# Kernel optimization log

Measured on AMD Instinct MI355X. Metric: run time of the kernel, lower is better.

Reference implementation:

```python
import jax, jax.numpy as jnp
import numpy as np

BATCH, SEQ, D_IN, D_HID, D_OUT = 256, 512, 128, 128, 128


def setup_inputs() -> dict:
    key = jax.random.key(0)
    ks = jax.random.split(key, 10)
    def xavier(k, shape):
        std = (2.0 / (shape[0] + shape[1])) ** 0.5
        return jax.random.normal(k, shape, dtype=jnp.float32) * std
    return {
        "x": jax.random.normal(ks[0], (BATCH, SEQ, D_IN), dtype=jnp.float32),
        "x2i": xavier(ks[1], (D_IN, D_HID)),
        "x2f": xavier(ks[2], (D_IN, D_HID)),
        "x2g": xavier(ks[3], (D_IN, D_HID)),
        "x2o": xavier(ks[4], (D_IN, D_HID)),
        "h2i": xavier(ks[5], (D_HID, D_HID)),
        "h2f": xavier(ks[6], (D_HID, D_HID)),
        "h2g": xavier(ks[7], (D_HID, D_HID)),
        "h2o": xavier(ks[8], (D_HID, D_HID)),
        "w_out": xavier(ks[9], (D_HID, D_OUT)),
    }


def reference(x, x2i, x2f, x2g, x2o, h2i, h2f, h2g, h2o, w_out):
    batch = x.shape[0]
    hid = h2i.shape[0]
    # Precompute input projections for all timesteps (same math, hoisted out
    # of the recurrence): [B, S, 4H] -> time-major [S, B, 4H]
    wx = jnp.concatenate([x2i, x2f, x2g, x2o], axis=1)       # [D_IN, 4H]
    wh = jnp.concatenate([h2i, h2f, h2g, h2o], axis=1)       # [H, 4H]
    xg = jnp.einsum("bsi,ik->sbk", x, wx)                    # [S, B, 4H]

    def step(carry, xg_t):
        c, h = carry
        gates = xg_t + h @ wh                                # [B, 4H]
        i = jax.nn.sigmoid(gates[:, 0 * hid:1 * hid])
        f = jax.nn.sigmoid(gates[:, 1 * hid:2 * hid])
        g = jnp.tanh(gates[:, 2 * hid:3 * hid])
        o = jax.nn.sigmoid(gates[:, 3 * hid:4 * hid])
        c = f * c + i * g
        h = o * jnp.tanh(c)
        return (c, h), None

    c0 = jnp.zeros((batch, hid), dtype=x.dtype)
    h0 = jnp.zeros((batch, hid), dtype=x.dtype)
    (c_T, h_T), _ = jax.lax.scan(step, (c0, h0), xg)
    return h_T @ w_out
```

## Files before the change

### kernel.cpp

```cpp
#include <hip/hip_runtime.h>

typedef unsigned int u32;
typedef __fp16 half2_t __attribute__((ext_vector_type(2)));
typedef __fp16 half8_t __attribute__((ext_vector_type(8)));
typedef float  f32x4   __attribute__((ext_vector_type(4)));

#define DIN 128
#define DH  128
#define SEQL 512
#define NBATCH 256
#define NC  512
#define TC  64
#define NCHUNK (SEQL/TC)

#define LDS_HOFF 65536
#define LDS_TOTAL (65536 + 512)

__device__ __forceinline__ u32 pk2(float a, float b) {
  half2_t h = __builtin_amdgcn_cvt_pkrtz(a, b);
  return __builtin_bit_cast(u32, h);
}

__device__ __forceinline__ float fexp2(float x) {
#if defined(__has_builtin) && __has_builtin(__builtin_amdgcn_exp2f)
  return __builtin_amdgcn_exp2f(x);
#else
  return __builtin_exp2f(x);
#endif
}

#define MF(A, B, C) __builtin_amdgcn_mfma_f32_16x16x32_f16( \
    __builtin_bit_cast(half8_t, A), __builtin_bit_cast(half8_t, B), C, 0, 0, 0)

__global__ void pack_w(const float* __restrict__ x2i, const float* __restrict__ x2f,
                       const float* __restrict__ x2g, const float* __restrict__ x2o,
                       const float* __restrict__ h2i, const float* __restrict__ h2f,
                       const float* __restrict__ h2g, const float* __restrict__ h2o,
                       u32* __restrict__ wxT, u32* __restrict__ whT) {
  int idx = blockIdx.x * blockDim.x + threadIdx.x;
  if (idx >= NC * 64) return;
  int j = idx >> 6, kk = idx & 63;
  int g = j >> 7, jjj = j & 127;
  const float* wx = (g == 0) ? x2i : (g == 1) ? x2f : (g == 2) ? x2g : x2o;
  const float* wh = (g == 0) ? h2i : (g == 1) ? h2f : (g == 2) ? h2g : h2o;
  wxT[idx] = pk2(wx[(2*kk)*DH + jjj], wx[(2*kk+1)*DH + jjj]);
  whT[idx] = pk2(wh[(2*kk)*DH + jjj], wh[(2*kk+1)*DH + jjj]);
}

__global__ __launch_bounds__(512, 2)
void lstm_fused(
    const float* __restrict__ x, const u32* __restrict__ wxT,
    const u32* __restrict__ whT, const float* __restrict__ w_out,
    float* __restrict__ out) {
  extern __shared__ char lds[];
  char* xgT = lds;

  const int tid = threadIdx.x;
  const int b   = blockIdx.x;
  const int l   = tid & 63, wv = tid >> 6;
  const int kg  = l >> 4, r15 = l & 15;

  uint4 bw[4][4];
#pragma unroll
  for (int g = 0; g < 4; ++g) {
    const uint4* wp = (const uint4*)(whT + (g * DH + wv * 16 + r15) * 64);
#pragma unroll
    for (int kt = 0; kt < 4; ++kt) bw[g][kt] = wp[kt * 4 + kg];
  }

  if (tid < 128) ((u32*)(lds + LDS_HOFF))[tid] = 0u;
  float c = 0.f;
  u32 rdh = LDS_HOFF;
  u32 wrh = LDS_HOFF + 256;
  const float* xb = x + (size_t)b * SEQL * DIN;
  __syncthreads();

  for (int ch = 0; ch < NCHUNK; ++ch) {
#pragma unroll 1
    for (int tt = 0; tt < 4; ++tt) {
      uint4 afr[4];
#pragma unroll
      for (int ko = 0; ko < 4; ++ko) {
        const float4* xp = (const float4*)(xb + (size_t)(ch*TC + tt*16 + r15)*DIN + ko*32 + kg*8);
        float4 v0 = xp[0], v1 = xp[1];
        afr[ko].x = pk2(v0.x, v0.y); afr[ko].y = pk2(v0.z, v0.w);
        afr[ko].z = pk2(v1.x, v1.y); afr[ko].w = pk2(v1.z, v1.w);
      }
#pragma unroll
      for (int nt = 0; nt < 4; ++nt) {
        int n = wv * 64 + nt * 16 + r15;
        f32x4 acc = {0.f, 0.f, 0.f, 0.f};
#pragma unroll
        for (int ko = 0; ko < 4; ++ko) {
          uint4 bf = *(const uint4*)(wxT + n*64 + ko*16 + kg*4);
          acc = MF(afr[ko], bf, acc);
        }
        int t0 = tt*16 + kg*4;
        u32 off = (u32)(n*128 + ((t0*2) ^ ((n & 7) << 4)));
        uint2 pw; pw.x = pk2(acc[0], acc[1]); pw.y = pk2(acc[2], acc[3]);
        *(uint2*)(xgT + off) = pw;
      }
    }
    __syncthreads();

#pragma unroll 1
    for (int m = 0; m < 8; ++m) {
      half8_t xh[4];
#pragma unroll
      for (int g = 0; g < 4; ++g) {
        int cg = g * DH + wv * 16 + r15;
        xh[g] = __builtin_bit_cast(half8_t,
            *(const uint4*)(xgT + cg*128 + ((m*16) ^ ((cg & 7) << 4))));
      }
#pragma unroll
      for (int s8 = 0; s8 < 8; ++s8) {
        uint4 a0 = *(const uint4*)(lds + rdh +   0 + kg*16);
        uint4 a1 = *(const uint4*)(lds + rdh +  64 + kg*16);
        uint4 a2 = *(const uint4*)(lds + rdh + 128 + kg*16);
        uint4 a3 = *(const uint4*)(lds + rdh + 192 + kg*16);
        f32x4 z = {0.f, 0.f, 0.f, 0.f};
        f32x4 aci = z, acf = z, acg = z, aco = z;
        aci = MF(a0, bw[0][0], aci); acf = MF(a0, bw[1][0], acf);
        acg = MF(a0, bw[2][0], acg); aco = MF(a0, bw[3][0], aco);
        aci = MF(a1, bw[0][1], aci); acf = MF(a1, bw[1][1], acf);
        acg = MF(a1, bw[2][1], acg); aco = MF(a1, bw[3][1], aco);
        aci = MF(a2, bw[0][2], aci); acf = MF(a2, bw[1][2], acf);
        acg = MF(a2, bw[2][2], acg); aco = MF(a2, bw[3][2], aco);
        aci = MF(a3, bw[0][3], aci); acf = MF(a3, bw[1][3], acf);
        acg = MF(a3, bw[2][3], acg); aco = MF(a3, bw[3][3], aco);
        float gi = aci[0] + (float)xh[0][s8];
        float gf = acf[0] + (float)xh[1][s8];
        float gg = acg[0] + (float)xh[2][s8];
        float go = aco[0] + (float)xh[3][s8];
        float si = __builtin_amdgcn_rcpf(1.f + fexp2(gi * -1.442695041f));
        float sf = __builtin_amdgcn_rcpf(1.f + fexp2(gf * -1.442695041f));
        float sg = __builtin_fmaf(2.f,
                     __builtin_amdgcn_rcpf(1.f + fexp2(gg * -2.885390082f)), -1.f);
        float so = __builtin_amdgcn_rcpf(1.f + fexp2(go * -1.442695041f));
        c = __builtin_fmaf(sf, c, si * sg);
        float th = __builtin_fmaf(2.f,
                     __builtin_amdgcn_rcpf(1.f + fexp2(c * -2.885390082f)), -1.f);
        float hval = so * th;
        if (l < 16) *(__fp16*)(lds + wrh + (wv * 16 + l) * 2) = (__fp16)hval;
        u32 tswap = rdh; rdh = wrh; wrh = tswap;
        __syncthreads();
      }
    }
  }

  if (tid < DH) {
    int n = tid;
    const u32* hf = (const u32*)(lds + rdh);
    float acc = 0.f;
#pragma unroll 8
    for (int kk = 0; kk < 64; ++kk) {
      half2_t h2v = __builtin_bit_cast(half2_t, hf[kk]);
      acc = __builtin_fmaf((float)h2v[0], w_out[(2*kk)*DH + n],
            __builtin_fmaf((float)h2v[1], w_out[(2*kk+1)*DH + n], acc));
    }
    out[b * DH + n] = acc;
  }
}

extern "C" void kernel_launch(void* const* d_in, const int* in_sizes, int n_in,
                              void* d_out, int out_size, void* d_ws, size_t ws_size,
                              hipStream_t stream) {
  const float* x    = (const float*)d_in[0];
  const float* x2i  = (const float*)d_in[1];
  const float* x2f  = (const float*)d_in[2];
  const float* x2g  = (const float*)d_in[3];
  const float* x2o  = (const float*)d_in[4];
  const float* h2i  = (const float*)d_in[5];
  const float* h2f  = (const float*)d_in[6];
  const float* h2g  = (const float*)d_in[7];
  const float* h2o  = (const float*)d_in[8];
  const float* wout = (const float*)d_in[9];

  u32* wxT = (u32*)d_ws;
  u32* whT = wxT + NC * 64;

  (void)hipFuncSetAttribute((const void*)lstm_fused,
                            hipFuncAttributeMaxDynamicSharedMemorySize, LDS_TOTAL);

  pack_w<<<64, 512, 0, stream>>>(x2i, x2f, x2g, x2o, h2i, h2f, h2g, h2o, wxT, whT);
  lstm_fused<<<NBATCH, 512, LDS_TOTAL, stream>>>(x, wxT, whT, wout, (float*)d_out);
}
```

Measured before the change: 288.7 us.

## Split recurrent matvec between MFMA waves and dot2 VALU waves

Waves 0-3 compute the i and f gates of the recurrent h@Wh product with MFMA, while waves 4-7 compute the g and o gates with packed fp16 dot2 instructions on the vector ALU. Partial gate sums are exchanged through a small LDS buffer, and the MFMA waves then apply the activations and write the new hidden state. The h buffer is no longer double-buffered, which adds a second barrier per timestep. This tries to balance matrix and vector units and shorten the per-step MFMA chain, at the cost of an extra synchronisation on the serial recurrence.

```diff
diff --git a/kernel.cpp b/kernel.cpp
--- a/kernel.cpp
+++ b/kernel.cpp
@@ -13,8 +13,9 @@
 #define TC  64
 #define NCHUNK (SEQL/TC)
 
-#define LDS_HOFF 65536
-#define LDS_TOTAL (65536 + 512)
+#define HOFF  65536
+#define GOFF  (65536 + 256)
+#define LDS_TOTAL (65536 + 256 + 2048)
 
 __device__ __forceinline__ u32 pk2(float a, float b) {
   half2_t h = __builtin_amdgcn_cvt_pkrtz(a, b);
@@ -26,6 +27,17 @@
   return __builtin_amdgcn_exp2f(x);
 #else
   return __builtin_exp2f(x);
+#endif
+}
+
+__device__ __forceinline__ float dot2(u32 a, u32 b, float c) {
+#if defined(__has_builtin) && __has_builtin(__builtin_amdgcn_fdot2)
+  return __builtin_amdgcn_fdot2(__builtin_bit_cast(half2_t, a),
+                                __builtin_bit_cast(half2_t, b), c, false);
+#else
+  half2_t ha = __builtin_bit_cast(half2_t, a);
+  half2_t hb = __builtin_bit_cast(half2_t, b);
+  return c + (float)ha[0]*(float)hb[0] + (float)ha[1]*(float)hb[1];
 #endif
 }
 
@@ -59,19 +71,29 @@
   const int b   = blockIdx.x;
   const int l   = tid & 63, wv = tid >> 6;
   const int kg  = l >> 4, r15 = l & 15;
-
-  uint4 bw[4][4];
-#pragma unroll
-  for (int g = 0; g < 4; ++g) {
-    const uint4* wp = (const uint4*)(whT + (g * DH + wv * 16 + r15) * 64);
-#pragma unroll
-    for (int kt = 0; kt < 4; ++kt) bw[g][kt] = wp[kt * 4 + kg];
+  const bool mfmaRole = (wv < 4);
+  const int ju  = (wv & 3) * 32 + (l & 31);
+  const int vix = wv - 4;
+  const int gslot = 2 + ((vix >> 1) & 1);
+  const int jv  = (vix & 1) * 64 + l;
+
+  uint4 wreg[16];
+  if (mfmaRole) {
+#pragma unroll
+    for (int t = 0; t < 4; ++t) {
+      int col = (t >> 1) * DH + (t & 1) * 64 + wv * 16 + r15;
+      const uint4* wp = (const uint4*)(whT + col * 64);
+#pragma unroll
+      for (int kt = 0; kt < 4; ++kt) wreg[t * 4 + kt] = wp[kt * 4 + kg];
+    }
+  } else {
+    const uint4* wp = (const uint4*)(whT + (gslot * DH + jv) * 64);
+#pragma unroll
+    for (int mm = 0; mm < 16; ++mm) wreg[mm] = wp[mm];
   }
 
-  if (tid < 128) ((u32*)(lds + LDS_HOFF))[tid] = 0u;
+  if (tid < 64) ((u32*)(lds + HOFF))[tid] = 0u;
   float c = 0.f;
-  u32 rdh = LDS_HOFF;
-  u32 wrh = LDS_HOFF + 256;
   const float* xb = x + (size_t)b * SEQL * DIN;
   __syncthreads();
 
@@ -106,43 +128,70 @@
 #pragma unroll 1
     for (int m = 0; m < 8; ++m) {
       half8_t xh[4];
-#pragma unroll
-      for (int g = 0; g < 4; ++g) {
-        int cg = g * DH + wv * 16 + r15;
-        xh[g] = __builtin_bit_cast(half8_t,
-            *(const uint4*)(xgT + cg*128 + ((m*16) ^ ((cg & 7) << 4))));
+      if (mfmaRole) {
+#pragma unroll
+        for (int g = 0; g < 4; ++g) {
+          int cg = g * DH + ju;
+          xh[g] = __builtin_bit_cast(half8_t,
+              *(const uint4*)(xgT + cg*128 + ((m*16) ^ ((cg & 7) << 4))));
+        }
       }
 #pragma unroll
       for (int s8 = 0; s8 < 8; ++s8) {
-        uint4 a0 = *(const uint4*)(lds + rdh +   0 + kg*16);
-        uint4 a1 = *(const uint4*)(lds + rdh +  64 + kg*16);
-        uint4 a2 = *(const uint4*)(lds + rdh + 128 + kg*16);
-        uint4 a3 = *(const uint4*)(lds + rdh + 192 + kg*16);
-        f32x4 z = {0.f, 0.f, 0.f, 0.f};
-        f32x4 aci = z, acf = z, acg = z, aco = z;
-        aci = MF(a0, bw[0][0], aci); acf = MF(a0, bw[1][0], acf);
-        acg = MF(a0, bw[2][0], acg); aco = MF(a0, bw[3][0], aco);
-        aci = MF(a1, bw[0][1], aci); acf = MF(a1, bw[1][1], acf);
-        acg = MF(a1, bw[2][1], acg); aco = MF(a1, bw[3][1], aco);
-        aci = MF(a2, bw[0][2], aci); acf = MF(a2, bw[1][2], acf);
-        acg = MF(a2, bw[2][2], acg); aco = MF(a2, bw[3][2], aco);
-        aci = MF(a3, bw[0][3], aci); acf = MF(a3, bw[1][3], acf);
-        acg = MF(a3, bw[2][3], acg); aco = MF(a3, bw[3][3], aco);
-        float gi = aci[0] + (float)xh[0][s8];
-        float gf = acf[0] + (float)xh[1][s8];
-        float gg = acg[0] + (float)xh[2][s8];
-        float go = aco[0] + (float)xh[3][s8];
-        float si = __builtin_amdgcn_rcpf(1.f + fexp2(gi * -1.442695041f));
-        float sf = __builtin_amdgcn_rcpf(1.f + fexp2(gf * -1.442695041f));
-        float sg = __builtin_fmaf(2.f,
-                     __builtin_amdgcn_rcpf(1.f + fexp2(gg * -2.885390082f)), -1.f);
-        float so = __builtin_amdgcn_rcpf(1.f + fexp2(go * -1.442695041f));
-        c = __builtin_fmaf(sf, c, si * sg);
-        float th = __builtin_fmaf(2.f,
-                     __builtin_amdgcn_rcpf(1.f + fexp2(c * -2.885390082f)), -1.f);
-        float hval = so * th;
-        if (l < 16) *(__fp16*)(lds + wrh + (wv * 16 + l) * 2) = (__fp16)hval;
-        u32 tswap = rdh; rdh = wrh; wrh = tswap;
+        if (mfmaRole) {
+          const char* hb = lds + HOFF + kg*16;
+          uint4 a0 = *(const uint4*)(hb);
+          uint4 a1 = *(const uint4*)(hb + 64);
+          uint4 a2 = *(const uint4*)(hb + 128);
+          uint4 a3 = *(const uint4*)(hb + 192);
+          f32x4 z = {0.f, 0.f, 0.f, 0.f};
+          f32x4 t0 = z, t1 = z, t2 = z, t3 = z;
+          t0 = MF(a0, wreg[0],  t0); t1 = MF(a0, wreg[4],  t1);
+          t2 = MF(a0, wreg[8],  t2); t3 = MF(a0, wreg[12], t3);
+          t0 = MF(a1, wreg[1],  t0); t1 = MF(a1, wreg[5],  t1);
+          t2 = MF(a1, wreg[9],  t2); t3 = MF(a1, wreg[13], t3);
+          t0 = MF(a2, wreg[2],  t0); t1 = MF(a2, wreg[6],  t1);
+          t2 = MF(a2, wreg[10], t2); t3 = MF(a2, wreg[14], t3);
+          t0 = MF(a3, wreg[3],  t0); t1 = MF(a3, wreg[7],  t1);
+          t2 = MF(a3, wreg[11], t2); t3 = MF(a3, wreg[15], t3);
+          if (kg == 0) {
+            int j0 = wv * 16 + r15, j1 = 64 + wv * 16 + r15;
+            float2 w0; w0.x = t0[0]; w0.y = t2[0];
+            float2 w1; w1.x = t1[0]; w1.y = t3[0];
+            *(float2*)(lds + GOFF + j0*16) = w0;
+            *(float2*)(lds + GOFF + j1*16) = w1;
+          }
+        } else {
+          const u32* hbv = (const u32*)(lds + HOFF);
+          float q0 = 0.f, q1 = 0.f, q2 = 0.f, q3 = 0.f;
+#pragma unroll
+          for (int mm = 0; mm < 16; ++mm) {
+            uint4 hv = *(const uint4*)(hbv + mm*4);
+            q0 = dot2(wreg[mm].x, hv.x, q0);
+            q1 = dot2(wreg[mm].y, hv.y, q1);
+            q2 = dot2(wreg[mm].z, hv.z, q2);
+            q3 = dot2(wreg[mm].w, hv.w, q3);
+          }
+          *(float*)(lds + GOFF + jv*16 + gslot*4) = (q0 + q1) + (q2 + q3);
+        }
+        __syncthreads();
+        if (mfmaRole) {
+          f32x4 gv = *(const f32x4*)(lds + GOFF + ju*16);
+          float gi = gv[0] + (float)xh[0][s8];
+          float gf = gv[1] + (float)xh[1][s8];
+          float gg = gv[2] + (float)xh[2][s8];
+          float go = gv[3] + (float)xh[3][s8];
+          float si = __builtin_amdgcn_rcpf(1.f + fexp2(gi * -1.442695041f));
+          float sf = __builtin_amdgcn_rcpf(1.f + fexp2(gf * -1.442695041f));
+          float sg = __builtin_fmaf(2.f,
+                       __builtin_amdgcn_rcpf(1.f + fexp2(gg * -2.885390082f)), -1.f);
+          float so = __builtin_amdgcn_rcpf(1.f + fexp2(go * -1.442695041f));
+          c = __builtin_fmaf(sf, c, si * sg);
+          float th = __builtin_fmaf(2.f,
+                       __builtin_amdgcn_rcpf(1.f + fexp2(c * -2.885390082f)), -1.f);
+          float hval = so * th;
+          if (l < 32) *(__fp16*)(lds + HOFF + ju*2) = (__fp16)hval;
+        }
         __syncthreads();
       }
     }
@@ -150,7 +199,7 @@
 
   if (tid < DH) {
     int n = tid;
-    const u32* hf = (const u32*)(lds + rdh);
+    const u32* hf = (const u32*)(lds + HOFF);
     float acc = 0.f;
 #pragma unroll 8
     for (int kk = 0; kk < 64; ++kk) {
```

Result: slower. 456.7 us (+58.2%).

## Double-buffer input projections and overlap next chunk with recurrence steps

Applied to the files above, without the earlier changes.

Adds a second LDS buffer for the per-chunk input projections. The next chunk's x loads and MFMA projection are interleaved into the current chunk's recurrence, with loads on even sub-blocks and compute plus store on odd ones, so the serial projection phase between chunks goes away. The per-step __syncthreads is replaced by a barrier that waits only on LDS counters, so in-flight global loads of x can stay outstanding across steps. LDS use doubles to about 128KB, which limits residency to one block per CU and adds register pressure from the held load values.

```diff
diff --git a/kernel.cpp b/kernel.cpp
--- a/kernel.cpp
+++ b/kernel.cpp
@@ -13,8 +13,8 @@
 #define TC  64
 #define NCHUNK (SEQL/TC)
 
-#define LDS_HOFF 65536
-#define LDS_TOTAL (65536 + 512)
+#define HOFF 131072
+#define LDS_TOTAL (131072 + 512)
 
 __device__ __forceinline__ u32 pk2(float a, float b) {
   half2_t h = __builtin_amdgcn_cvt_pkrtz(a, b);
@@ -27,6 +27,12 @@
 #else
   return __builtin_exp2f(x);
 #endif
+}
+
+__device__ __forceinline__ void step_barrier() {
+  asm volatile("s_waitcnt lgkmcnt(0)" ::: "memory");
+  __builtin_amdgcn_s_barrier();
+  asm volatile("" ::: "memory");
 }
 
 #define MF(A, B, C) __builtin_amdgcn_mfma_f32_16x16x32_f16( \
@@ -53,65 +59,108 @@
     const u32* __restrict__ whT, const float* __restrict__ w_out,
     float* __restrict__ out) {
   extern __shared__ char lds[];
-  char* xgT = lds;
 
   const int tid = threadIdx.x;
   const int b   = blockIdx.x;
   const int l   = tid & 63, wv = tid >> 6;
   const int kg  = l >> 4, r15 = l & 15;
+  const int j   = wv * 16 + r15;
 
   uint4 bw[4][4];
 #pragma unroll
   for (int g = 0; g < 4; ++g) {
-    const uint4* wp = (const uint4*)(whT + (g * DH + wv * 16 + r15) * 64);
+    const uint4* wp = (const uint4*)(whT + (g * DH + j) * 64);
 #pragma unroll
     for (int kt = 0; kt < 4; ++kt) bw[g][kt] = wp[kt * 4 + kg];
   }
 
-  if (tid < 128) ((u32*)(lds + LDS_HOFF))[tid] = 0u;
+  if (tid < 128) ((u32*)(lds + HOFF))[tid] = 0u;
   float c = 0.f;
-  u32 rdh = LDS_HOFF;
-  u32 wrh = LDS_HOFF + 256;
+  u32 rdh = HOFF;
+  u32 wrh = HOFF + 256;
   const float* xb = x + (size_t)b * SEQL * DIN;
   __syncthreads();
 
+#pragma unroll 1
+  for (int tt = 0; tt < 4; ++tt) {
+    uint4 afr[4];
+#pragma unroll
+    for (int ko = 0; ko < 4; ++ko) {
+      const float4* xp = (const float4*)(xb + (size_t)(tt*16 + r15)*DIN + ko*32 + kg*8);
+      float4 v0 = xp[0], v1 = xp[1];
+      afr[ko].x = pk2(v0.x, v0.y); afr[ko].y = pk2(v0.z, v0.w);
+      afr[ko].z = pk2(v1.x, v1.y); afr[ko].w = pk2(v1.z, v1.w);
+    }
+#pragma unroll
+    for (int nt = 0; nt < 4; ++nt) {
+      int n = wv * 64 + nt * 16 + r15;
+      f32x4 acc = {0.f, 0.f, 0.f, 0.f};
+#pragma unroll
+      for (int ko = 0; ko < 4; ++ko) {
+        uint4 bf = *(const uint4*)(wxT + n*64 + ko*16 + kg*4);
+        acc = MF(afr[ko], bf, acc);
+      }
+      int t0 = tt*16 + kg*4;
+      u32 off = (u32)(n*128 + ((t0*2) ^ ((n & 7) << 4)));
+      uint2 pw; pw.x = pk2(acc[0], acc[1]); pw.y = pk2(acc[2], acc[3]);
+      *(uint2*)(lds + off) = pw;
+    }
+  }
+  __syncthreads();
+
+  int cur = 0;
+#pragma unroll 1
   for (int ch = 0; ch < NCHUNK; ++ch) {
-#pragma unroll 1
-    for (int tt = 0; tt < 4; ++tt) {
-      uint4 afr[4];
-#pragma unroll
-      for (int ko = 0; ko < 4; ++ko) {
-        const float4* xp = (const float4*)(xb + (size_t)(ch*TC + tt*16 + r15)*DIN + ko*32 + kg*8);
-        float4 v0 = xp[0], v1 = xp[1];
-        afr[ko].x = pk2(v0.x, v0.y); afr[ko].y = pk2(v0.z, v0.w);
-        afr[ko].z = pk2(v1.x, v1.y); afr[ko].w = pk2(v1.z, v1.w);
-      }
-#pragma unroll
-      for (int nt = 0; nt < 4; ++nt) {
-        int n = wv * 64 + nt * 16 + r15;
-        f32x4 acc = {0.f, 0.f, 0.f, 0.f};
-#pragma unroll
-        for (int ko = 0; ko < 4; ++ko) {
-          uint4 bf = *(const uint4*)(wxT + n*64 + ko*16 + kg*4);
-          acc = MF(afr[ko], bf, acc);
-        }
-        int t0 = tt*16 + kg*4;
-        u32 off = (u32)(n*128 + ((t0*2) ^ ((n & 7) << 4)));
-        uint2 pw; pw.x = pk2(acc[0], acc[1]); pw.y = pk2(acc[2], acc[3]);
-        *(uint2*)(xgT + off) = pw;
-      }
-    }
-    __syncthreads();
+    char* xgC = lds + cur * 65536;
+    char* xgN = lds + (cur ^ 1) * 65536;
+    const bool doA = (ch + 1 < NCHUNK);
+    float4 lv[8];
 
 #pragma unroll 1
     for (int m = 0; m < 8; ++m) {
       half8_t xh[4];
 #pragma unroll
       for (int g = 0; g < 4; ++g) {
-        int cg = g * DH + wv * 16 + r15;
+        int cg = g * DH + j;
         xh[g] = __builtin_bit_cast(half8_t,
-            *(const uint4*)(xgT + cg*128 + ((m*16) ^ ((cg & 7) << 4))));
-      }
+            *(const uint4*)(xgC + cg*128 + ((m*16) ^ ((cg & 7) << 4))));
+      }
+
+      if (doA) {
+        int tt = m >> 1;
+        if ((m & 1) == 0) {
+          const float* xr = xb + (size_t)((ch+1)*TC + tt*16 + r15)*DIN + kg*8;
+#pragma unroll
+          for (int ko = 0; ko < 4; ++ko) {
+            const float4* xp = (const float4*)(xr + ko*32);
+            lv[2*ko]   = xp[0];
+            lv[2*ko+1] = xp[1];
+          }
+        } else {
+          uint4 afr[4];
+#pragma unroll
+          for (int ko = 0; ko < 4; ++ko) {
+            float4 v0 = lv[2*ko], v1 = lv[2*ko+1];
+            afr[ko].x = pk2(v0.x, v0.y); afr[ko].y = pk2(v0.z, v0.w);
+            afr[ko].z = pk2(v1.x, v1.y); afr[ko].w = pk2(v1.z, v1.w);
+          }
+#pragma unroll
+          for (int nt = 0; nt < 4; ++nt) {
+            int n = wv * 64 + nt * 16 + r15;
+            f32x4 acc = {0.f, 0.f, 0.f, 0.f};
+#pragma unroll
+            for (int ko = 0; ko < 4; ++ko) {
+              uint4 bf = *(const uint4*)(wxT + n*64 + ko*16 + kg*4);
+              acc = MF(afr[ko], bf, acc);
+            }
+            int t0 = tt*16 + kg*4;
+            u32 off = (u32)(n*128 + ((t0*2) ^ ((n & 7) << 4)));
+            uint2 pw; pw.x = pk2(acc[0], acc[1]); pw.y = pk2(acc[2], acc[3]);
+            *(uint2*)(xgN + off) = pw;
+          }
+        }
+      }
+
 #pragma unroll
       for (int s8 = 0; s8 < 8; ++s8) {
         uint4 a0 = *(const uint4*)(lds + rdh +   0 + kg*16);
@@ -141,11 +190,12 @@
         float th = __builtin_fmaf(2.f,
                      __builtin_amdgcn_rcpf(1.f + fexp2(c * -2.885390082f)), -1.f);
         float hval = so * th;
-        if (l < 16) *(__fp16*)(lds + wrh + (wv * 16 + l) * 2) = (__fp16)hval;
-        u32 tswap = rdh; rdh = wrh; wrh = tswap;
-        __syncthreads();
-      }
-    }
+        if (l < 16) *(__fp16*)(lds + wrh + j * 2) = (__fp16)hval;
+        step_barrier();
+        rdh ^= 256; wrh ^= 256;
+      }
+    }
+    cur ^= 1;
   }
 
   if (tid < DH) {
```

Result: slower. 340.3 us (+17.9%).
